# Performance work log

Measured on AMD Instinct MI355X. Metric: run time of the kernel, lower is better.

## Reference

```python
import jax, jax.numpy as jnp
import numpy as np

B, T, N = 256, 512, 128
GO, EOS = 1, 2  # mead-baseline Offsets
NEG = -10000.0


def setup_inputs() -> dict:
    key = jax.random.key(0)
    k1, k2, k3 = jax.random.split(key, 3)
    unaries = jax.random.normal(k1, (B, T, N), dtype=jnp.float32)
    # constraint mask: True where transition is INVALID (masked to -1e4)
    cmask = jax.random.bernoulli(k2, 0.3, (1, N, N))
    trans = jax.nn.log_softmax(
        jnp.where(cmask, jnp.float32(NEG), jnp.float32(0.0)), axis=1
    )  # [1, N, N], matches buffer construction in __init__
    lengths = jax.random.randint(k3, (B,), T // 2, T + 1).astype(jnp.int64)
    lengths = lengths.at[0].set(T)  # ensure max(lengths) == T
    return {"unaries": unaries, "trans": trans, "lengths": lengths}


def _viterbi(probv, trans, lengths, start_idx, end_idx):
    # probv: [T, B, N] log-probs; trans: [1, N, N]; lengths: [B]
    seq_len, batch, n_tags = probv.shape
    trans0 = trans[0]  # [N(cur), N(prev)]
    lengths = lengths.astype(jnp.int32)

    alphas = jnp.full((batch, n_tags), NEG, probv.dtype).at[:, start_idx].set(0.0)
    alphas = jax.nn.log_softmax(alphas, axis=-1)

    def step(alphas, xs):
        unary_t, i = xs  # [B, N], scalar
        ntv = alphas[:, None, :] + trans0[None]          # [B, N_cur, N_prev]
        bp = jnp.argmax(ntv, axis=2)                     # backpointers [B, N]
        new_alphas = jnp.max(ntv, axis=2) + unary_t      # [B, N]
        alphas = jnp.where((i < lengths)[:, None], new_alphas, alphas)
        return alphas, bp

    alphas, bps = jax.lax.scan(step, alphas, (probv, jnp.arange(seq_len)))

    terminal = alphas + trans0[end_idx][None, :]         # [B, N]
    path_score = jnp.max(terminal, axis=1)               # [B]
    best_tag = jnp.argmax(terminal, axis=1)              # [B]

    rev_len = seq_len - lengths - 1

    def back(btid, xs):
        bp, i = xs  # bp: [B, N]
        new = jnp.take_along_axis(bp, btid[:, None], axis=1)[:, 0]
        btid = jnp.where(i > rev_len, new, btid)
        return btid, btid

    _, ys = jax.lax.scan(back, best_tag, (bps[::-1], jnp.arange(seq_len)))
    full = jnp.concatenate([best_tag[None], ys], axis=0)  # [T+1, B]
    best_path = full[:seq_len][::-1]                       # [T, B]

    seq_mask = jnp.arange(seq_len)[:, None] < lengths[None, :]  # [T, B]
    best_path = jnp.where(seq_mask, best_path, 0)
    return best_path, path_score


def reference(unaries, trans, lengths):
    # constrained branch of TaggerGreedyDecoder.forward (batch_first=True)
    probv = jax.nn.log_softmax(jnp.swapaxes(unaries, 0, 1), axis=-1)  # [T,B,N]
    preds_tb, scores = _viterbi(probv, trans, lengths, GO, EOS)
    return jnp.swapaxes(preds_tb, 0, 1), scores  # ([B,T], [B])
```

## Files before the change

kernel.cpp:

```cpp
#include <hip/hip_runtime.h>

#define BB 256
#define TT 512
#define NN 128
#define GO_IDX 1
#define EOS_IDX 2
#define TSPLIT 368
#define NEGV (-10000.0f)
#define ASLOT(x) ((x) + (((x) >> 5) << 2))

#define STEP_BARRIER() asm volatile("s_waitcnt lgkmcnt(0)\n\ts_barrier" ::: "memory")

__device__ __forceinline__ float dpp_xor1_f(float x) {
    return __int_as_float(__builtin_amdgcn_update_dpp(0, __float_as_int(x), 0xB1, 0xF, 0xF, true));
}
__device__ __forceinline__ float dpp_xor2_f(float x) {
    return __int_as_float(__builtin_amdgcn_update_dpp(0, __float_as_int(x), 0x4E, 0xF, 0xF, true));
}
__device__ __forceinline__ int dpp_xor1_i(int x) {
    return __builtin_amdgcn_update_dpp(0, x, 0xB1, 0xF, 0xF, true);
}
__device__ __forceinline__ int dpp_xor2_i(int x) {
    return __builtin_amdgcn_update_dpp(0, x, 0x4E, 0xF, 0xF, true);
}

template <int USE_WS>
__global__ __launch_bounds__(512) void viterbi_kernel(
    float* __restrict__ u,
    const float* __restrict__ trans,
    const int*   __restrict__ lengths_raw,
    float* __restrict__ out,
    unsigned char* __restrict__ ws)
{
    __shared__ unsigned char bps[(TSPLIT - 1) * NN];
    __shared__ __align__(16) float prob[2][16][NN];
    __shared__ __align__(16) float alpha[2][144];
    __shared__ float fin_v[2];
    __shared__ int   fin_i[2];

    const int tid  = threadIdx.x;
    const int b    = blockIdx.x;
    const int wave = tid >> 6;
    const int lane = tid & 63;
    const int q    = tid & 3;
    const int cur  = tid >> 2;
    const int hw   = tid >> 5;
    const int l32  = tid & 31;

    int len;
    {
        int probe = lengths_raw[1];
        len = (probe == 0) ? lengths_raw[2 * b] : lengths_raw[b];
    }

    float* pb = u + (size_t)b * TT * NN;
    const float4* pb4 = (const float4*)pb;
    unsigned char* spb = USE_WS ? (ws + (size_t)b * ((TT - TSPLIT) * NN)) : (unsigned char*)pb;

    float tr[32];
    {
        const float4* t4 = (const float4*)(trans + cur * NN + q * 32);
#pragma unroll
        for (int i = 0; i < 8; ++i) {
            float4 v = t4[i];
            tr[4*i+0] = v.x; tr[4*i+1] = v.y; tr[4*i+2] = v.z; tr[4*i+3] = v.w;
        }
    }

    if (tid < NN) alpha[0][ASLOT(tid)] = (tid == GO_IDX) ? 0.0f : NEGV;

    auto normrow = [&](float4 v, float* dstrow) {
        float m = fmaxf(fmaxf(v.x, v.y), fmaxf(v.z, v.w));
#pragma unroll
        for (int off = 16; off; off >>= 1) m = fmaxf(m, __shfl_xor(m, off, 64));
        float s = expf(v.x - m) + expf(v.y - m) + expf(v.z - m) + expf(v.w - m);
#pragma unroll
        for (int off = 16; off; off >>= 1) s += __shfl_xor(s, off, 64);
        float ls = logf(s);
        ((float4*)dstrow)[l32] =
            make_float4((v.x - m) - ls, (v.y - m) - ls, (v.z - m) - ls, (v.w - m) - ls);
    };

    float4 R = pb4[hw * 32 + l32];
    normrow(R, &prob[0][hw][0]);
    R = pb4[(16 + hw) * 32 + l32];
    __syncthreads();

    const int nG = (len + 15) >> 4;
    for (int g = 0; g < nG; ++g) {
        const int tb = g << 4;
        normrow(R, &prob[(g + 1) & 1][hw][0]);
        {
            int rr = tb + 32 + hw;
            if (rr > TT - 1) rr = TT - 1;
            R = pb4[rr * 32 + l32];
        }
#pragma unroll 4
        for (int k = 0; k < 16; ++k) {
            const int t = tb + k;
            if (t < len) {
                const float Pv = prob[g & 1][k][cur];
                const float* ra = alpha[t & 1];
                float*       wa = alpha[(t & 1) ^ 1];
                const float4* a4 = (const float4*)(ra + q * 36);
                float bv[4]; int bi[4];
#pragma unroll
                for (int c = 0; c < 4; ++c) {
                    float4 a0 = a4[c * 2], a1 = a4[c * 2 + 1];
                    const int base = c * 8;
                    bv[c] = a0.x + tr[base + 0]; bi[c] = base + 0;
                    float x;
                    x = a0.y + tr[base + 1]; if (x > bv[c]) { bv[c] = x; bi[c] = base + 1; }
                    x = a0.z + tr[base + 2]; if (x > bv[c]) { bv[c] = x; bi[c] = base + 2; }
                    x = a0.w + tr[base + 3]; if (x > bv[c]) { bv[c] = x; bi[c] = base + 3; }
                    x = a1.x + tr[base + 4]; if (x > bv[c]) { bv[c] = x; bi[c] = base + 4; }
                    x = a1.y + tr[base + 5]; if (x > bv[c]) { bv[c] = x; bi[c] = base + 5; }
                    x = a1.z + tr[base + 6]; if (x > bv[c]) { bv[c] = x; bi[c] = base + 6; }
                    x = a1.w + tr[base + 7]; if (x > bv[c]) { bv[c] = x; bi[c] = base + 7; }
                }
                float best = bv[0]; int bp = bi[0];
#pragma unroll
                for (int c = 1; c < 4; ++c) { if (bv[c] > best) { best = bv[c]; bp = bi[c]; } }
                bp += q * 32;

                float v1 = dpp_xor1_f(best); int b1 = dpp_xor1_i(bp);
                bool  t1 = (q & 1) ? (v1 >= best) : (v1 > best);
                float m1 = t1 ? v1 : best;   int p1 = t1 ? b1 : bp;
                float v2 = dpp_xor2_f(m1);   int b2 = dpp_xor2_i(p1);
                bool  t2 = (q & 2) ? (v2 >= m1) : (v2 > m1);
                float M  = t2 ? v2 : m1;     int BP = t2 ? b2 : p1;

                if (q == 0) {
                    wa[ASLOT(cur)] = M + Pv;
                    if (t >= 1) {
                        if (t < TSPLIT) bps[(t - 1) * NN + cur] = (unsigned char)BP;
                        else if (USE_WS) spb[(t - TSPLIT) * NN + cur] = (unsigned char)BP;
                        else             spb[(size_t)t * 512 + cur] = (unsigned char)BP;
                    }
                }
                STEP_BARRIER();
            }
        }
    }

    __threadfence();

    if (tid < NN) {
        float v = alpha[len & 1][ASLOT(tid)] + trans[EOS_IDX * NN + tid];
        int idx = tid;
#pragma unroll
        for (int off = 32; off; off >>= 1) {
            float ov = __shfl_xor(v, off, 64);
            int   oi = __shfl_xor(idx, off, 64);
            if (ov > v || (ov == v && oi < idx)) { v = ov; idx = oi; }
        }
        if (lane == 0) { fin_v[wave] = v; fin_i[wave] = idx; }
    }
    __syncthreads();

    const int lenU = __builtin_amdgcn_readfirstlane(len);

    for (int t = lenU + tid; t < TT; t += 512) out[(size_t)b * TT + t] = 0.0f;

    {
        unsigned int* cache = (unsigned int*)&prob[0][0][0];
        const volatile unsigned int* src = (const volatile unsigned int*)spb;
        for (int i = tid; i < 128 * 32; i += 512) {
            if (USE_WS) cache[i] = src[(size_t)(i >> 5) * 32 + (i & 31)];
            else        cache[i] = src[(size_t)(TSPLIT + (i >> 5)) * 128 + (i & 31)];
        }
    }
    __syncthreads();

    float sc; int T0;
    {
        float v0 = fin_v[0], v1 = fin_v[1];
        int   i0 = fin_i[0], i1 = fin_i[1];
        if (v1 > v0) { sc = v1; T0 = i1; }
        else         { sc = v0; T0 = i0; }
    }
    if (tid == 0) {
        out[(size_t)BB * TT + b] = sc;
        out[(size_t)b * TT + (lenU - 1)] = (float)T0;
    }

    const unsigned char* cacheb = (const unsigned char*)&prob[0][0][0];
    unsigned char* lt   = (unsigned char*)&alpha[0][0];
    unsigned char* Harr = lt + 1024;

    const int s  = wave;
    const int A  = lenU - 1 - 64 * s;
    const int h0 = lane;
    const int h1 = 64 + lane;
    const int Jmax = (A < 64) ? A : 64;

    unsigned int rec0[16], rec1[16];
#pragma unroll
    for (int i = 0; i < 16; ++i) { rec0[i] = 0u; rec1[i] = 0u; }

    int c0 = h0, c1 = h1;
#pragma unroll
    for (int j = 1; j <= 64; ++j) {
        if (j <= Jmax) {
            const int x = A - j + 1;
            int n0, n1;
            if (x < TSPLIT) {
                n0 = bps[(x - 1) * NN + c0];
                n1 = bps[(x - 1) * NN + c1];
            } else if (x < TSPLIT + 128) {
                n0 = cacheb[(x - TSPLIT) * NN + c0];
                n1 = cacheb[(x - TSPLIT) * NN + c1];
            } else {
                if (USE_WS) {
                    n0 = ((const volatile unsigned char*)spb)[(size_t)(x - TSPLIT) * NN + c0];
                    n1 = ((const volatile unsigned char*)spb)[(size_t)(x - TSPLIT) * NN + c1];
                } else {
                    n0 = ((const volatile unsigned char*)spb)[(size_t)x * 512 + c0];
                    n1 = ((const volatile unsigned char*)spb)[(size_t)x * 512 + c1];
                }
            }
            c0 = n0; c1 = n1;
            rec0[(j - 1) >> 2] |= (unsigned int)c0 << (((j - 1) & 3) * 8);
            rec1[(j - 1) >> 2] |= (unsigned int)c1 << (((j - 1) & 3) * 8);
        }
    }
    if (A >= 65) {
        lt[s * NN + h0] = (unsigned char)c0;
        lt[s * NN + h1] = (unsigned char)c1;
    }
    __syncthreads();

    if (tid == 0) {
        int H = T0;
        Harr[0] = (unsigned char)H;
#pragma unroll
        for (int ss = 1; ss < 8; ++ss) {
            if (lenU - 1 - 64 * ss >= 1) {
                H = lt[(ss - 1) * NN + H];
                Harr[ss] = (unsigned char)H;
            }
        }
    }
    __syncthreads();

    if (A >= 1) {
        const int Hs = Harr[s];
        if (h0 == Hs) {
#pragma unroll
            for (int j = 1; j <= 64; ++j)
                if (j <= Jmax)
                    out[(size_t)b * TT + (A - j)] =
                        (float)((rec0[(j - 1) >> 2] >> (((j - 1) & 3) * 8)) & 255u);
        }
        if (h1 == Hs) {
#pragma unroll
            for (int j = 1; j <= 64; ++j)
                if (j <= Jmax)
                    out[(size_t)b * TT + (A - j)] =
                        (float)((rec1[(j - 1) >> 2] >> (((j - 1) & 3) * 8)) & 255u);
        }
    }
}

extern "C" void kernel_launch(void* const* d_in, const int* in_sizes, int n_in,
                              void* d_out, int out_size, void* d_ws, size_t ws_size,
                              hipStream_t stream) {
    float*       unaries = (float*)d_in[0];
    const float* trans   = (const float*)d_in[1];
    const int*   lengths = (const int*)d_in[2];
    float* out = (float*)d_out;
    unsigned char* ws = (unsigned char*)d_ws;

    const size_t need = (size_t)BB * (TT - TSPLIT) * NN;
    if (ws != nullptr && ws_size >= need) {
        hipLaunchKernelGGL(HIP_KERNEL_NAME(viterbi_kernel<1>), dim3(BB), dim3(512), 0, stream,
                           unaries, trans, lengths, out, ws);
    } else {
        hipLaunchKernelGGL(HIP_KERNEL_NAME(viterbi_kernel<0>), dim3(BB), dim3(512), 0, stream,
                           unaries, trans, lengths, out, ws);
    }
}
```

Measured before the change: 473.1 us.

## Pack two batch sequences per 1024-thread block and shrink LDS backpointer split

Each block now processes two batch elements with 512 threads apiece, so the grid halves to 128 blocks of 1024 threads. The per-step barrier is shared across both sequences and runs up to the longer of the two lengths. To fit two sets of backpointers in LDS, the in-LDS split drops from 368 to 180 steps. Later steps' backpointers are always written into the consumed region of the unaries buffer, and the workspace path is removed. The aim is to hide per-step latency by running more waves per CU. The cost is idle CUs, heavier barriers, and more global traffic during the backtrace.

```diff
diff --git a/kernel.cpp b/kernel.cpp
--- a/kernel.cpp
+++ b/kernel.cpp
@@ -5,7 +5,7 @@
 #define NN 128
 #define GO_IDX 1
 #define EOS_IDX 2
-#define TSPLIT 368
+#define TSPLIT 180
 #define NEGV (-10000.0f)
 #define ASLOT(x) ((x) + (((x) >> 5) << 2))
 
@@ -24,38 +24,39 @@
     return __builtin_amdgcn_update_dpp(0, x, 0x4E, 0xF, 0xF, true);
 }
 
-template <int USE_WS>
-__global__ __launch_bounds__(512) void viterbi_kernel(
+__global__ __launch_bounds__(1024) void viterbi_kernel(
     float* __restrict__ u,
     const float* __restrict__ trans,
     const int*   __restrict__ lengths_raw,
-    float* __restrict__ out,
-    unsigned char* __restrict__ ws)
+    float* __restrict__ out)
 {
-    __shared__ unsigned char bps[(TSPLIT - 1) * NN];
-    __shared__ __align__(16) float prob[2][16][NN];
-    __shared__ __align__(16) float alpha[2][144];
-    __shared__ float fin_v[2];
-    __shared__ int   fin_i[2];
+    __shared__ unsigned char bps[2][(TSPLIT - 1) * NN];
+    __shared__ __align__(16) float prob[2][2][8][NN];
+    __shared__ __align__(16) float alpha[2][2][144];
+    __shared__ float fin_v[2][2];
+    __shared__ int   fin_i[2][2];
+    __shared__ int   len_sh[2];
 
     const int tid  = threadIdx.x;
-    const int b    = blockIdx.x;
-    const int wave = tid >> 6;
-    const int lane = tid & 63;
-    const int q    = tid & 3;
-    const int cur  = tid >> 2;
-    const int hw   = tid >> 5;
-    const int l32  = tid & 31;
+    const int bi   = tid >> 9;
+    const int lt   = tid & 511;
+    const int b    = (blockIdx.x << 1) | bi;
+    const int wv   = lt >> 6;
+    const int lane = lt & 63;
+    const int q    = lt & 3;
+    const int cur  = lt >> 2;
+    const int hwr  = lt >> 5;
+    const int l32  = lt & 31;
 
     int len;
     {
         int probe = lengths_raw[1];
         len = (probe == 0) ? lengths_raw[2 * b] : lengths_raw[b];
     }
+    if (lt == 0) len_sh[bi] = len;
 
     float* pb = u + (size_t)b * TT * NN;
     const float4* pb4 = (const float4*)pb;
-    unsigned char* spb = USE_WS ? (ws + (size_t)b * ((TT - TSPLIT) * NN)) : (unsigned char*)pb;
 
     float tr[32];
     {
@@ -67,7 +68,7 @@
         }
     }
 
-    if (tid < NN) alpha[0][ASLOT(tid)] = (tid == GO_IDX) ? 0.0f : NEGV;
+    if (lt < NN) alpha[bi][0][ASLOT(lt)] = (lt == GO_IDX) ? 0.0f : NEGV;
 
     auto normrow = [&](float4 v, float* dstrow) {
         float m = fmaxf(fmaxf(v.x, v.y), fmaxf(v.z, v.w));
@@ -81,46 +82,50 @@
             make_float4((v.x - m) - ls, (v.y - m) - ls, (v.z - m) - ls, (v.w - m) - ls);
     };
 
-    float4 R = pb4[hw * 32 + l32];
-    normrow(R, &prob[0][hw][0]);
-    R = pb4[(16 + hw) * 32 + l32];
-    __syncthreads();
-
-    const int nG = (len + 15) >> 4;
+    float4 R;
+    if (lt < 256) {
+        R = pb4[hwr * 32 + l32];
+        normrow(R, &prob[bi][0][hwr][0]);
+        R = pb4[(8 + hwr) * 32 + l32];
+    }
+    __syncthreads();
+
+    const int lenmax = max(len_sh[0], len_sh[1]);
+    const int nG = (lenmax + 7) >> 3;
     for (int g = 0; g < nG; ++g) {
-        const int tb = g << 4;
-        normrow(R, &prob[(g + 1) & 1][hw][0]);
-        {
-            int rr = tb + 32 + hw;
+        const int tb = g << 3;
+        if (lt < 256) {
+            normrow(R, &prob[bi][(g + 1) & 1][hwr][0]);
+            int rr = tb + 16 + hwr;
             if (rr > TT - 1) rr = TT - 1;
             R = pb4[rr * 32 + l32];
         }
 #pragma unroll 4
-        for (int k = 0; k < 16; ++k) {
+        for (int k = 0; k < 8; ++k) {
             const int t = tb + k;
             if (t < len) {
-                const float Pv = prob[g & 1][k][cur];
-                const float* ra = alpha[t & 1];
-                float*       wa = alpha[(t & 1) ^ 1];
+                const float Pv = prob[bi][g & 1][k][cur];
+                const float* ra = alpha[bi][t & 1];
+                float*       wa = alpha[bi][(t & 1) ^ 1];
                 const float4* a4 = (const float4*)(ra + q * 36);
-                float bv[4]; int bi[4];
+                float bv[4]; int bi4[4];
 #pragma unroll
                 for (int c = 0; c < 4; ++c) {
                     float4 a0 = a4[c * 2], a1 = a4[c * 2 + 1];
                     const int base = c * 8;
-                    bv[c] = a0.x + tr[base + 0]; bi[c] = base + 0;
+                    bv[c] = a0.x + tr[base + 0]; bi4[c] = base + 0;
                     float x;
-                    x = a0.y + tr[base + 1]; if (x > bv[c]) { bv[c] = x; bi[c] = base + 1; }
-                    x = a0.z + tr[base + 2]; if (x > bv[c]) { bv[c] = x; bi[c] = base + 2; }
-                    x = a0.w + tr[base + 3]; if (x > bv[c]) { bv[c] = x; bi[c] = base + 3; }
-                    x = a1.x + tr[base + 4]; if (x > bv[c]) { bv[c] = x; bi[c] = base + 4; }
-                    x = a1.y + tr[base + 5]; if (x > bv[c]) { bv[c] = x; bi[c] = base + 5; }
-                    x = a1.z + tr[base + 6]; if (x > bv[c]) { bv[c] = x; bi[c] = base + 6; }
-                    x = a1.w + tr[base + 7]; if (x > bv[c]) { bv[c] = x; bi[c] = base + 7; }
+                    x = a0.y + tr[base + 1]; if (x > bv[c]) { bv[c] = x; bi4[c] = base + 1; }
+                    x = a0.z + tr[base + 2]; if (x > bv[c]) { bv[c] = x; bi4[c] = base + 2; }
+                    x = a0.w + tr[base + 3]; if (x > bv[c]) { bv[c] = x; bi4[c] = base + 3; }
+                    x = a1.x + tr[base + 4]; if (x > bv[c]) { bv[c] = x; bi4[c] = base + 4; }
+                    x = a1.y + tr[base + 5]; if (x > bv[c]) { bv[c] = x; bi4[c] = base + 5; }
+                    x = a1.z + tr[base + 6]; if (x > bv[c]) { bv[c] = x; bi4[c] = base + 6; }
+                    x = a1.w + tr[base + 7]; if (x > bv[c]) { bv[c] = x; bi4[c] = base + 7; }
                 }
-                float best = bv[0]; int bp = bi[0];
-#pragma unroll
-                for (int c = 1; c < 4; ++c) { if (bv[c] > best) { best = bv[c]; bp = bi[c]; } }
+                float best = bv[0]; int bp = bi4[0];
+#pragma unroll
+                for (int c = 1; c < 4; ++c) { if (bv[c] > best) { best = bv[c]; bp = bi4[c]; } }
                 bp += q * 32;
 
                 float v1 = dpp_xor1_f(best); int b1 = dpp_xor1_i(bp);
@@ -133,62 +138,59 @@
                 if (q == 0) {
                     wa[ASLOT(cur)] = M + Pv;
                     if (t >= 1) {
-                        if (t < TSPLIT) bps[(t - 1) * NN + cur] = (unsigned char)BP;
-                        else if (USE_WS) spb[(t - TSPLIT) * NN + cur] = (unsigned char)BP;
-                        else             spb[(size_t)t * 512 + cur] = (unsigned char)BP;
+                        if (t < TSPLIT) bps[bi][(t - 1) * NN + cur] = (unsigned char)BP;
+                        else ((unsigned char*)pb)[(size_t)t * 512 + cur] = (unsigned char)BP;
                     }
                 }
-                STEP_BARRIER();
             }
+            STEP_BARRIER();
         }
     }
 
     __threadfence();
 
-    if (tid < NN) {
-        float v = alpha[len & 1][ASLOT(tid)] + trans[EOS_IDX * NN + tid];
-        int idx = tid;
+    if (lt < NN) {
+        float v = alpha[bi][len & 1][ASLOT(lt)] + trans[EOS_IDX * NN + lt];
+        int idx = lt;
 #pragma unroll
         for (int off = 32; off; off >>= 1) {
             float ov = __shfl_xor(v, off, 64);
             int   oi = __shfl_xor(idx, off, 64);
             if (ov > v || (ov == v && oi < idx)) { v = ov; idx = oi; }
         }
-        if (lane == 0) { fin_v[wave] = v; fin_i[wave] = idx; }
+        if (lane == 0) { fin_v[bi][wv] = v; fin_i[bi][wv] = idx; }
     }
     __syncthreads();
 
     const int lenU = __builtin_amdgcn_readfirstlane(len);
 
-    for (int t = lenU + tid; t < TT; t += 512) out[(size_t)b * TT + t] = 0.0f;
-
-    {
-        unsigned int* cache = (unsigned int*)&prob[0][0][0];
-        const volatile unsigned int* src = (const volatile unsigned int*)spb;
-        for (int i = tid; i < 128 * 32; i += 512) {
-            if (USE_WS) cache[i] = src[(size_t)(i >> 5) * 32 + (i & 31)];
-            else        cache[i] = src[(size_t)(TSPLIT + (i >> 5)) * 128 + (i & 31)];
-        }
+    for (int t = lenU + lt; t < TT; t += 512) out[(size_t)b * TT + t] = 0.0f;
+
+    {
+        unsigned int* cache = (unsigned int*)&prob[bi][0][0][0];
+        const volatile unsigned int* src = (const volatile unsigned int*)pb;
+        for (int i = lt; i < 64 * 32; i += 512)
+            cache[i] = src[(size_t)(TSPLIT + (i >> 5)) * 128 + (i & 31)];
     }
     __syncthreads();
 
     float sc; int T0;
     {
-        float v0 = fin_v[0], v1 = fin_v[1];
-        int   i0 = fin_i[0], i1 = fin_i[1];
+        float v0 = fin_v[bi][0], v1 = fin_v[bi][1];
+        int   i0 = fin_i[bi][0], i1 = fin_i[bi][1];
         if (v1 > v0) { sc = v1; T0 = i1; }
         else         { sc = v0; T0 = i0; }
     }
-    if (tid == 0) {
+    if (lt == 0) {
         out[(size_t)BB * TT + b] = sc;
         out[(size_t)b * TT + (lenU - 1)] = (float)T0;
     }
 
-    const unsigned char* cacheb = (const unsigned char*)&prob[0][0][0];
-    unsigned char* lt   = (unsigned char*)&alpha[0][0];
-    unsigned char* Harr = lt + 1024;
-
-    const int s  = wave;
+    const unsigned char* cacheb = (const unsigned char*)&prob[bi][0][0][0];
+    unsigned char* lt_tab = (unsigned char*)&alpha[bi][0][0];
+    unsigned char* Harr   = lt_tab + 1024;
+
+    const int s  = wv;
     const int A  = lenU - 1 - 64 * s;
     const int h0 = lane;
     const int h1 = 64 + lane;
@@ -205,19 +207,14 @@
             const int x = A - j + 1;
             int n0, n1;
             if (x < TSPLIT) {
-                n0 = bps[(x - 1) * NN + c0];
-                n1 = bps[(x - 1) * NN + c1];
-            } else if (x < TSPLIT + 128) {
+                n0 = bps[bi][(x - 1) * NN + c0];
+                n1 = bps[bi][(x - 1) * NN + c1];
+            } else if (x < TSPLIT + 64) {
                 n0 = cacheb[(x - TSPLIT) * NN + c0];
                 n1 = cacheb[(x - TSPLIT) * NN + c1];
             } else {
-                if (USE_WS) {
-                    n0 = ((const volatile unsigned char*)spb)[(size_t)(x - TSPLIT) * NN + c0];
-                    n1 = ((const volatile unsigned char*)spb)[(size_t)(x - TSPLIT) * NN + c1];
-                } else {
-                    n0 = ((const volatile unsigned char*)spb)[(size_t)x * 512 + c0];
-                    n1 = ((const volatile unsigned char*)spb)[(size_t)x * 512 + c1];
-                }
+                n0 = ((const volatile unsigned char*)pb)[(size_t)x * 512 + c0];
+                n1 = ((const volatile unsigned char*)pb)[(size_t)x * 512 + c1];
             }
             c0 = n0; c1 = n1;
             rec0[(j - 1) >> 2] |= (unsigned int)c0 << (((j - 1) & 3) * 8);
@@ -225,18 +222,18 @@
         }
     }
     if (A >= 65) {
-        lt[s * NN + h0] = (unsigned char)c0;
-        lt[s * NN + h1] = (unsigned char)c1;
-    }
-    __syncthreads();
-
-    if (tid == 0) {
+        lt_tab[s * NN + h0] = (unsigned char)c0;
+        lt_tab[s * NN + h1] = (unsigned char)c1;
+    }
+    __syncthreads();
+
+    if (lt == 0) {
         int H = T0;
         Harr[0] = (unsigned char)H;
 #pragma unroll
         for (int ss = 1; ss < 8; ++ss) {
             if (lenU - 1 - 64 * ss >= 1) {
-                H = lt[(ss - 1) * NN + H];
+                H = lt_tab[(ss - 1) * NN + H];
                 Harr[ss] = (unsigned char)H;
             }
         }
@@ -269,14 +266,8 @@
     const float* trans   = (const float*)d_in[1];
     const int*   lengths = (const int*)d_in[2];
     float* out = (float*)d_out;
-    unsigned char* ws = (unsigned char*)d_ws;
-
-    const size_t need = (size_t)BB * (TT - TSPLIT) * NN;
-    if (ws != nullptr && ws_size >= need) {
-        hipLaunchKernelGGL(HIP_KERNEL_NAME(viterbi_kernel<1>), dim3(BB), dim3(512), 0, stream,
-                           unaries, trans, lengths, out, ws);
-    } else {
-        hipLaunchKernelGGL(HIP_KERNEL_NAME(viterbi_kernel<0>), dim3(BB), dim3(512), 0, stream,
-                           unaries, trans, lengths, out, ws);
-    }
-}
+    (void)d_ws; (void)ws_size; (void)in_sizes; (void)n_in; (void)out_size;
+
+    hipLaunchKernelGGL(viterbi_kernel, dim3(BB / 2), dim3(1024), 0, stream,
+                       unaries, trans, lengths, out);
+}
```

Result: slower. 658.6 us (+39.2%).

## Split block into compute and loader warps, each compute thread handling two tags

Applied to the files above, without the earlier changes.

The block is now split in two. Threads 0-255 do the Viterbi max/argmax recurrence, each computing two current tags (cp and cp+64) from a single shared read of alpha. Threads 256-511 handle prefetching and log-softmax normalisation of the unary rows. This takes the normalisation work and global loads off the critical recurrence path and halves the number of waves doing the per-step compute. In exchange, each compute thread does twice the arithmetic and needs more registers for two transition rows.

```diff
diff --git a/kernel.cpp b/kernel.cpp
--- a/kernel.cpp
+++ b/kernel.cpp
@@ -21,7 +21,7 @@
     return __builtin_amdgcn_update_dpp(0, x, 0xB1, 0xF, 0xF, true);
 }
 __device__ __forceinline__ int dpp_xor2_i(int x) {
-    return __builtin_amdgcn_update_dpp(0, x, 0x4E, 0xF, 0xF, true);
+    return __int_as_float(0), __builtin_amdgcn_update_dpp(0, x, 0x4E, 0xF, 0xF, true);
 }
 
 template <int USE_WS>
@@ -40,11 +40,12 @@
 
     const int tid  = threadIdx.x;
     const int b    = blockIdx.x;
-    const int wave = tid >> 6;
+    const int wv   = tid >> 6;
     const int lane = tid & 63;
+    const bool comp = (tid < 256);
     const int q    = tid & 3;
-    const int cur  = tid >> 2;
-    const int hw   = tid >> 5;
+    const int cp   = (tid & 255) >> 2;
+    const int hw2  = (tid & 255) >> 5;
     const int l32  = tid & 31;
 
     int len;
@@ -57,13 +58,16 @@
     const float4* pb4 = (const float4*)pb;
     unsigned char* spb = USE_WS ? (ws + (size_t)b * ((TT - TSPLIT) * NN)) : (unsigned char*)pb;
 
-    float tr[32];
-    {
-        const float4* t4 = (const float4*)(trans + cur * NN + q * 32);
+    float trA[32], trB[32];
+    if (comp) {
+        const float4* tA = (const float4*)(trans + cp * NN + q * 32);
+        const float4* tB = (const float4*)(trans + (cp + 64) * NN + q * 32);
 #pragma unroll
         for (int i = 0; i < 8; ++i) {
-            float4 v = t4[i];
-            tr[4*i+0] = v.x; tr[4*i+1] = v.y; tr[4*i+2] = v.z; tr[4*i+3] = v.w;
+            float4 va = tA[i];
+            trA[4*i+0] = va.x; trA[4*i+1] = va.y; trA[4*i+2] = va.z; trA[4*i+3] = va.w;
+            float4 vb = tB[i];
+            trB[4*i+0] = vb.x; trB[4*i+1] = vb.y; trB[4*i+2] = vb.z; trB[4*i+3] = vb.w;
         }
     }
 
@@ -81,61 +85,83 @@
             make_float4((v.x - m) - ls, (v.y - m) - ls, (v.z - m) - ls, (v.w - m) - ls);
     };
 
-    float4 R = pb4[hw * 32 + l32];
-    normrow(R, &prob[0][hw][0]);
-    R = pb4[(16 + hw) * 32 + l32];
+    auto curchain = [&](const float4* av, const float* tr, float& Mo, int& BPo) {
+        float bv[4]; int bi4[4];
+#pragma unroll
+        for (int c = 0; c < 4; ++c) {
+            float4 a0 = av[c * 2], a1 = av[c * 2 + 1];
+            const int base = c * 8;
+            bv[c] = a0.x + tr[base + 0]; bi4[c] = base + 0;
+            float x;
+            x = a0.y + tr[base + 1]; if (x > bv[c]) { bv[c] = x; bi4[c] = base + 1; }
+            x = a0.z + tr[base + 2]; if (x > bv[c]) { bv[c] = x; bi4[c] = base + 2; }
+            x = a0.w + tr[base + 3]; if (x > bv[c]) { bv[c] = x; bi4[c] = base + 3; }
+            x = a1.x + tr[base + 4]; if (x > bv[c]) { bv[c] = x; bi4[c] = base + 4; }
+            x = a1.y + tr[base + 5]; if (x > bv[c]) { bv[c] = x; bi4[c] = base + 5; }
+            x = a1.z + tr[base + 6]; if (x > bv[c]) { bv[c] = x; bi4[c] = base + 6; }
+            x = a1.w + tr[base + 7]; if (x > bv[c]) { bv[c] = x; bi4[c] = base + 7; }
+        }
+        float best = bv[0]; int bp = bi4[0];
+#pragma unroll
+        for (int c = 1; c < 4; ++c) { if (bv[c] > best) { best = bv[c]; bp = bi4[c]; } }
+        bp += q * 32;
+
+        float v1 = dpp_xor1_f(best); int b1 = dpp_xor1_i(bp);
+        bool  t1 = (q & 1) ? (v1 >= best) : (v1 > best);
+        float m1 = t1 ? v1 : best;   int p1 = t1 ? b1 : bp;
+        float v2 = dpp_xor2_f(m1);   int b2 = dpp_xor2_i(p1);
+        bool  t2 = (q & 2) ? (v2 >= m1) : (v2 > m1);
+        Mo  = t2 ? v2 : m1;          BPo = t2 ? b2 : p1;
+    };
+
+    float4 R0, R1;
+    if (!comp) {
+        R0 = pb4[hw2 * 32 + l32];
+        R1 = pb4[(8 + hw2) * 32 + l32];
+        normrow(R0, &prob[0][hw2][0]);
+        normrow(R1, &prob[0][hw2 + 8][0]);
+        R0 = pb4[(16 + hw2) * 32 + l32];
+        R1 = pb4[(24 + hw2) * 32 + l32];
+    }
     __syncthreads();
 
     const int nG = (len + 15) >> 4;
     for (int g = 0; g < nG; ++g) {
         const int tb = g << 4;
-        normrow(R, &prob[(g + 1) & 1][hw][0]);
-        {
-            int rr = tb + 32 + hw;
-            if (rr > TT - 1) rr = TT - 1;
-            R = pb4[rr * 32 + l32];
+        if (!comp) {
+            normrow(R0, &prob[(g + 1) & 1][hw2][0]);
+            normrow(R1, &prob[(g + 1) & 1][hw2 + 8][0]);
+            int r0 = tb + 32 + hw2;     if (r0 > TT - 1) r0 = TT - 1;
+            int r1 = tb + 32 + 8 + hw2; if (r1 > TT - 1) r1 = TT - 1;
+            R0 = pb4[r0 * 32 + l32];
+            R1 = pb4[r1 * 32 + l32];
         }
 #pragma unroll 4
         for (int k = 0; k < 16; ++k) {
             const int t = tb + k;
             if (t < len) {
-                const float Pv = prob[g & 1][k][cur];
-                const float* ra = alpha[t & 1];
-                float*       wa = alpha[(t & 1) ^ 1];
-                const float4* a4 = (const float4*)(ra + q * 36);
-                float bv[4]; int bi[4];
-#pragma unroll
-                for (int c = 0; c < 4; ++c) {
-                    float4 a0 = a4[c * 2], a1 = a4[c * 2 + 1];
-                    const int base = c * 8;
-                    bv[c] = a0.x + tr[base + 0]; bi[c] = base + 0;
-                    float x;
-                    x = a0.y + tr[base + 1]; if (x > bv[c]) { bv[c] = x; bi[c] = base + 1; }
-                    x = a0.z + tr[base + 2]; if (x > bv[c]) { bv[c] = x; bi[c] = base + 2; }
-                    x = a0.w + tr[base + 3]; if (x > bv[c]) { bv[c] = x; bi[c] = base + 3; }
-                    x = a1.x + tr[base + 4]; if (x > bv[c]) { bv[c] = x; bi[c] = base + 4; }
-                    x = a1.y + tr[base + 5]; if (x > bv[c]) { bv[c] = x; bi[c] = base + 5; }
-                    x = a1.z + tr[base + 6]; if (x > bv[c]) { bv[c] = x; bi[c] = base + 6; }
-                    x = a1.w + tr[base + 7]; if (x > bv[c]) { bv[c] = x; bi[c] = base + 7; }
-                }
-                float best = bv[0]; int bp = bi[0];
-#pragma unroll
-                for (int c = 1; c < 4; ++c) { if (bv[c] > best) { best = bv[c]; bp = bi[c]; } }
-                bp += q * 32;
-
-                float v1 = dpp_xor1_f(best); int b1 = dpp_xor1_i(bp);
-                bool  t1 = (q & 1) ? (v1 >= best) : (v1 > best);
-                float m1 = t1 ? v1 : best;   int p1 = t1 ? b1 : bp;
-                float v2 = dpp_xor2_f(m1);   int b2 = dpp_xor2_i(p1);
-                bool  t2 = (q & 2) ? (v2 >= m1) : (v2 > m1);
-                float M  = t2 ? v2 : m1;     int BP = t2 ? b2 : p1;
-
-                if (q == 0) {
-                    wa[ASLOT(cur)] = M + Pv;
-                    if (t >= 1) {
-                        if (t < TSPLIT) bps[(t - 1) * NN + cur] = (unsigned char)BP;
-                        else if (USE_WS) spb[(t - TSPLIT) * NN + cur] = (unsigned char)BP;
-                        else             spb[(size_t)t * 512 + cur] = (unsigned char)BP;
+                if (comp) {
+                    const float Pv = prob[g & 1][k][(q & 1) ? cp + 64 : cp];
+                    const float* ra = alpha[t & 1];
+                    float*       wa = alpha[(t & 1) ^ 1];
+                    const float4* a4 = (const float4*)(ra + q * 36);
+                    float4 av[8];
+#pragma unroll
+                    for (int i = 0; i < 8; ++i) av[i] = a4[i];
+
+                    float Ma, Mb; int BPa, BPb;
+                    curchain(av, trA, Ma, BPa);
+                    curchain(av, trB, Mb, BPb);
+
+                    const bool isB = q & 1;
+                    const int  curw = isB ? cp + 64 : cp;
+                    if (q < 2) {
+                        wa[ASLOT(curw)] = (isB ? Mb : Ma) + Pv;
+                    } else if (t >= 1) {
+                        const int BPw = isB ? BPb : BPa;
+                        if (t < TSPLIT) bps[(t - 1) * NN + curw] = (unsigned char)BPw;
+                        else if (USE_WS) spb[(t - TSPLIT) * NN + curw] = (unsigned char)BPw;
+                        else             spb[(size_t)t * 512 + curw] = (unsigned char)BPw;
                     }
                 }
                 STEP_BARRIER();
@@ -154,7 +180,7 @@
             int   oi = __shfl_xor(idx, off, 64);
             if (ov > v || (ov == v && oi < idx)) { v = ov; idx = oi; }
         }
-        if (lane == 0) { fin_v[wave] = v; fin_i[wave] = idx; }
+        if (lane == 0) { fin_v[wv] = v; fin_i[wv] = idx; }
     }
     __syncthreads();
 
@@ -188,7 +214,7 @@
     unsigned char* lt   = (unsigned char*)&alpha[0][0];
     unsigned char* Harr = lt + 1024;
 
-    const int s  = wave;
+    const int s  = wv;
     const int A  = lenU - 1 - 64 * s;
     const int h0 = lane;
     const int h1 = 64 + lane;
```

Measured after the change: 574.6 us. 21.4% more time.
